# Kernel tuning notes

Hardware: AMD Instinct MI355X
Metric: run time of the kernel (lower is better)

## Reference

```python
import jax, jax.numpy as jnp
import numpy as np

D_MODEL = 1024
NUM_HEADS = 16
D_K = D_MODEL // NUM_HEADS  # 64
THETA = 10000.0
B = 2
L = 2048


def _rope(x, positions):
    # x: [B, H, L, d_k], positions: [B, L]
    half = D_K // 2
    freqs = 1.0 / (THETA ** (jnp.arange(0, D_K, 2, dtype=jnp.float32) / D_K))  # [half]
    angles = positions.astype(jnp.float32)[..., None] * freqs  # [B, L, half]
    cos = jnp.cos(angles)[:, None, :, :]  # [B, 1, L, half]
    sin = jnp.sin(angles)[:, None, :, :]
    x_even = x[..., 0::2]
    x_odd = x[..., 1::2]
    r_even = x_even * cos - x_odd * sin
    r_odd = x_even * sin + x_odd * cos
    # interleave back: [..., half, 2] -> [..., d_k]
    return jnp.stack([r_even, r_odd], axis=-1).reshape(x.shape)


def setup_inputs() -> dict:
    key = jax.random.key(0)
    ks = jax.random.split(key, 5)
    std = np.sqrt(2.0 / (D_MODEL + D_MODEL))
    x = jax.random.normal(ks[0], (B, L, D_MODEL), dtype=jnp.float32)
    token_positions = jnp.broadcast_to(jnp.arange(L, dtype=jnp.int64 if jax.config.jax_enable_x64 else jnp.int32), (B, L))
    WQ = jax.random.truncated_normal(ks[1], -3.0, 3.0, (D_MODEL, D_MODEL), dtype=jnp.float32) * std
    WK = jax.random.truncated_normal(ks[2], -3.0, 3.0, (D_MODEL, D_MODEL), dtype=jnp.float32) * std
    WV = jax.random.truncated_normal(ks[3], -3.0, 3.0, (D_MODEL, D_MODEL), dtype=jnp.float32) * std
    WO = jax.random.truncated_normal(ks[4], -3.0, 3.0, (D_MODEL, D_MODEL), dtype=jnp.float32) * std
    return {"x": x, "token_positions": token_positions, "WQ": WQ, "WK": WK, "WV": WV, "WO": WO}


def reference(x, token_positions, WQ, WK, WV, WO):
    # Projections: W is [out, in] -> y = x @ W.T
    Q = jnp.einsum('bld,ed->ble', x, WQ)
    K = jnp.einsum('bld,ed->ble', x, WK)
    V = jnp.einsum('bld,ed->ble', x, WV)
    # [B, L, H*d] -> [B, H, L, d]
    def split_heads(t):
        return t.reshape(B, L, NUM_HEADS, D_K).transpose(0, 2, 1, 3)
    Q, K, V = split_heads(Q), split_heads(K), split_heads(V)
    Q = _rope(Q, token_positions)
    K = _rope(K, token_positions)
    scores = jnp.einsum('bhqd,bhkd->bhqk', Q, K) / np.sqrt(D_K).astype(np.float32)
    causal = jnp.tril(jnp.ones((L, L), dtype=bool))
    scores = jnp.where(causal, scores, -jnp.inf)
    attn = jax.nn.softmax(scores, axis=-1)
    out = jnp.einsum('bhqk,bhkd->bhqd', attn, V)  # [B, H, L, d]
    out = out.transpose(0, 2, 1, 3).reshape(B, L, D_MODEL)
    return jnp.einsum('bld,ed->ble', out, WO)
```

## Files before the change

kernel.cpp:

```cpp
#include <hip/hip_runtime.h>
#include <cstdint>
#include <cstddef>

#define D_MODEL 1024
#define NHEAD   16
#define DKH     64
#define BATCH   2
#define SEQ     2048
#define BL      (BATCH*SEQ)

typedef unsigned short u16;
typedef unsigned int   u32;
typedef __bf16 bf16_t;
typedef bf16_t bf16x8 __attribute__((ext_vector_type(8)));
typedef u16    u16x8  __attribute__((ext_vector_type(8)));
typedef u32    u32x4  __attribute__((ext_vector_type(4)));
typedef float  f32x4  __attribute__((ext_vector_type(4)));
typedef float  f32x16 __attribute__((ext_vector_type(16)));

__device__ __forceinline__ u16 f2bf(float f) {
  u32 u = __builtin_bit_cast(u32, f);
  u32 r = (u + 0x7FFFu + ((u >> 16) & 1u)) >> 16;
  return (u16)r;
}
__device__ __forceinline__ float bf2f(u16 h) {
  u32 u = ((u32)h) << 16;
  return __builtin_bit_cast(float, u);
}
__device__ __forceinline__ bf16x8 ldb8(const u16* p) {
  return __builtin_bit_cast(bf16x8, *(const u16x8*)p);
}
__device__ __forceinline__ void gl_lds16(const u16* g, u16* l) {
  __builtin_amdgcn_global_load_lds((const __attribute__((address_space(1))) void*)g,
                                   (__attribute__((address_space(3))) void*)l, 16, 0, 0);
}
#define MFMA16x16x32(a,b,c) __builtin_amdgcn_mfma_f32_16x16x32_bf16((a),(b),(c),0,0,0)
#define MFMA32x32x16(a,b,c) __builtin_amdgcn_mfma_f32_32x32x16_bf16((a),(b),(c),0,0,0)

__global__ void __launch_bounds__(256) cvt1_kernel(const float* __restrict__ in, u16* __restrict__ out, int n8) {
  int i = blockIdx.x * 256 + threadIdx.x;
  if (i >= n8) return;
  float4 a = ((const float4*)in)[2*i];
  float4 b = ((const float4*)in)[2*i+1];
  u16x8 o;
  o[0]=f2bf(a.x); o[1]=f2bf(a.y); o[2]=f2bf(a.z); o[3]=f2bf(a.w);
  o[4]=f2bf(b.x); o[5]=f2bf(b.y); o[6]=f2bf(b.z); o[7]=f2bf(b.w);
  ((u16x8*)out)[i] = o;
}

__global__ void __launch_bounds__(256) cvt4_kernel(const float* __restrict__ i0, const float* __restrict__ i1,
                                                   const float* __restrict__ i2, const float* __restrict__ i3,
                                                   u16* __restrict__ o0, u16* __restrict__ o1,
                                                   u16* __restrict__ o2, u16* __restrict__ o3, int n8) {
  int i = blockIdx.x * 256 + threadIdx.x;
  if (i >= n8) return;
  const float* in = (blockIdx.y == 0) ? i0 : (blockIdx.y == 1) ? i1 : (blockIdx.y == 2) ? i2 : i3;
  u16*        out = (blockIdx.y == 0) ? o0 : (blockIdx.y == 1) ? o1 : (blockIdx.y == 2) ? o2 : o3;
  float4 a = ((const float4*)in)[2*i];
  float4 b = ((const float4*)in)[2*i+1];
  u16x8 o;
  o[0]=f2bf(a.x); o[1]=f2bf(a.y); o[2]=f2bf(a.z); o[3]=f2bf(a.w);
  o[4]=f2bf(b.x); o[5]=f2bf(b.y); o[6]=f2bf(b.z); o[7]=f2bf(b.w);
  ((u16x8*)out)[i] = o;
}

template<bool F32OUT>
__device__ __forceinline__ void gemm_body(const u16* __restrict__ A, const u16* __restrict__ W,
                                          void* __restrict__ Cv, int M, int N, int K,
                                          const int* __restrict__ pos, int mode) {
  __shared__ u16 Als[128*64];
  __shared__ u16 Bls[128*64];
  const int tid = threadIdx.x, lane = tid & 63, w = tid >> 6;
  const int wr = w >> 1, wc = w & 1;
  const int lr = lane & 15, lg = lane >> 4;
  const int m0 = blockIdx.x * 128, n0 = blockIdx.y * 128;
  f32x4 acc[4][4] = {};
  const int srow = lane >> 3;
  const int scol = (lane & 7) * 8;
  for (int k0 = 0; k0 < K; k0 += 64) {
    __syncthreads();
    #pragma unroll
    for (int c = 0; c < 4; ++c) {
      const int rb = w*32 + c*8;
      const u16* ga = A + (size_t)(m0 + rb + srow)*K + k0 + scol;
      const u16* gb = W + (size_t)(n0 + rb + srow)*K + k0 + scol;
      gl_lds16(ga, &Als[rb*64]);
      gl_lds16(gb, &Bls[rb*64]);
    }
    __syncthreads();
    #pragma unroll
    for (int ks = 0; ks < 2; ++ks) {
      bf16x8 am[4], bn[4];
      #pragma unroll
      for (int f = 0; f < 4; ++f) {
        am[f] = ldb8(&Als[(wr*64 + f*16 + lr)*64 + ks*32 + lg*8]);
        bn[f] = ldb8(&Bls[(wc*64 + f*16 + lr)*64 + ks*32 + lg*8]);
      }
      #pragma unroll
      for (int fm = 0; fm < 4; ++fm)
        #pragma unroll
        for (int fn = 0; fn < 4; ++fn)
          acc[fm][fn] = MFMA16x16x32(am[fm], bn[fn], acc[fm][fn]);
    }
  }
  if constexpr (!F32OUT) {
    if (mode) {
      const float QS  = 0.18033688011112042f;
      const float sgn = (lane & 1) ? 1.0f : -1.0f;
      float fr[4];
      #pragma unroll
      for (int fn = 0; fn < 4; ++fn)
        fr[fn] = exp2f(-(float)((fn*16 + lr) >> 1) * 0.41524101186092f);
      #pragma unroll
      for (int fm = 0; fm < 4; ++fm)
        #pragma unroll
        for (int r = 0; r < 4; ++r) {
          const int row = m0 + wr*64 + fm*16 + lg*4 + r;
          const float p = (float)pos[row];
          #pragma unroll
          for (int fn = 0; fn < 4; ++fn) {
            float sv, cv;
            __sincosf(p * fr[fn], &sv, &cv);
            float v  = acc[fm][fn][r];
            float vp = __shfl_xor(v, 1, 64);
            float out = v*cv + sgn*vp*sv;
            if (mode == 1) out *= QS;
            ((u16*)Cv)[(size_t)row*N + n0 + wc*64 + fn*16 + lr] = f2bf(out);
          }
        }
      return;
    }
  }
  #pragma unroll
  for (int fm = 0; fm < 4; ++fm)
    #pragma unroll
    for (int fn = 0; fn < 4; ++fn)
      #pragma unroll
      for (int r = 0; r < 4; ++r) {
        const int row = m0 + wr*64 + fm*16 + lg*4 + r;
        const int col = n0 + wc*64 + fn*16 + lr;
        if constexpr (F32OUT) ((float*)Cv)[(size_t)row*N + col] = acc[fm][fn][r];
        else                  ((u16*)Cv)[(size_t)row*N + col] = f2bf(acc[fm][fn][r]);
      }
}

__global__ void __launch_bounds__(256) gemm_qkv_kernel(const u16* __restrict__ X,
    const u16* __restrict__ Wq, const u16* __restrict__ Wk, const u16* __restrict__ Wv,
    u16* __restrict__ Qo, u16* __restrict__ Ko, u16* __restrict__ Vo,
    const int* __restrict__ pos) {
  const u16* W = (blockIdx.z == 0) ? Wq : (blockIdx.z == 1) ? Wk : Wv;
  u16*       C = (blockIdx.z == 0) ? Qo : (blockIdx.z == 1) ? Ko : Vo;
  const int mode = (blockIdx.z == 0) ? 1 : (blockIdx.z == 1) ? 2 : 0;
  gemm_body<false>(X, W, C, BL, D_MODEL, D_MODEL, pos, mode);
}

__global__ void __launch_bounds__(256) gemm_out_kernel(const u16* __restrict__ A, const u16* __restrict__ W,
                                                       float* __restrict__ C) {
  gemm_body<true>(A, W, C, BL, D_MODEL, D_MODEL, nullptr, 0);
}


struct AttnLds {
  union {
    struct { u16 K[2][2][64*64]; u16 V[2][2][64*64]; } s;
    float mg[4*64*34];
  } u;
};

__device__ __forceinline__ void attn_pass(
    const int q0, const int T,
    const u16* __restrict__ Qb, const u16* __restrict__ Kb,
    const u16* __restrict__ Vb, u16* __restrict__ Ob,
    AttnLds& sh, const int lane, const int w)
{
  const int wl = w & 3, isB = w >> 2;
  const int l31 = lane & 31, h32 = lane >> 5;
  const int SPLIT = T >> 1;
  const int qw0 = q0 + wl * 32;
  const int srow  = lane >> 3;
  const int scol8 = ((lane & 7) ^ srow) * 8;
  const int t0 = isB ? SPLIT : 0;
  const int vswz = (l31 & 7) << 3;

  bf16x8 qf[4];
  #pragma unroll
  for (int kc = 0; kc < 4; ++kc)
    qf[kc] = ldb8(Qb + (size_t)(qw0 + l31)*D_MODEL + kc*16 + h32*8);
  f32x16 o0 = {}, o1 = {};
  float mrun = 0.0f, lrun = 0.0f;

  {
    const int kv = t0 * 64;
    #pragma unroll
    for (int c = 0; c < 2; ++c) {
      const int rb = wl*16 + c*8;
      gl_lds16(Kb + (size_t)(kv + rb + srow)*D_MODEL + scol8, &sh.u.s.K[isB][0][rb*64]);
    }
    u16x8 a = *(const u16x8*)(Vb + (size_t)(kv + lane)*D_MODEL + (wl*2)*8);
    u16x8 c = *(const u16x8*)(Vb + (size_t)(kv + lane)*D_MODEL + (wl*2+1)*8);
    #pragma unroll
    for (int j = 0; j < 8; ++j) sh.u.s.V[isB][0][(wl*16 + j)*64 + (lane ^ (j<<3))] = a[j];
    #pragma unroll
    for (int j = 0; j < 8; ++j) sh.u.s.V[isB][0][(wl*16 + 8 + j)*64 + (lane ^ (j<<3))] = c[j];
  }
  __syncthreads();

  for (int i = 0; i < SPLIT; ++i) {
    const int buf = i & 1, nbuf = buf ^ 1;
    const bool pf = (i + 1 < SPLIT);
    u16x8 vr0, vr1;
    if (pf) {
      const int kvn = (t0 + i + 1) * 64;
      #pragma unroll
      for (int c = 0; c < 2; ++c) {
        const int rb = wl*16 + c*8;
        gl_lds16(Kb + (size_t)(kvn + rb + srow)*D_MODEL + scol8, &sh.u.s.K[isB][nbuf][rb*64]);
      }
      vr0 = *(const u16x8*)(Vb + (size_t)(kvn + lane)*D_MODEL + (wl*2)*8);
      vr1 = *(const u16x8*)(Vb + (size_t)(kvn + lane)*D_MODEL + (wl*2+1)*8);
    }
    const int kv0 = (t0 + i) * 64;
    if (kv0 <= qw0 + 31) {
      const u16* K0 = sh.u.s.K[isB][buf];
      const u16* V0 = sh.u.s.V[isB][buf];
      f32x16 s[2];
      #pragma unroll
      for (int r = 0; r < 16; ++r) { s[0][r] = -mrun; s[1][r] = -mrun; }
      #pragma unroll
      for (int kc = 0; kc < 4; ++kc) {
        const int sl = ((2*kc + h32) ^ (l31 & 7)) * 8;
        bf16x8 k0 = ldb8(&K0[(l31)*64 + sl]);
        bf16x8 k1 = ldb8(&K0[(32 + l31)*64 + sl]);
        s[0] = MFMA32x32x16(k0, qf[kc], s[0]);
        s[1] = MFMA32x32x16(k1, qf[kc], s[1]);
      }
      if (kv0 + 63 > qw0) {
        const int qrow = qw0 + l31;
        #pragma unroll
        for (int kb = 0; kb < 2; ++kb)
          #pragma unroll
          for (int r = 0; r < 16; ++r) {
            int kp = kv0 + kb*32 + (r&3) + 8*(r>>2) + 4*h32;
            if (kp > qrow) s[kb][r] = -1e30f;
          }
      }
      float t[16];
      #pragma unroll
      for (int j = 0; j < 16; ++j) t[j] = fmaxf(s[0][j], s[1][j]);
      #pragma unroll
      for (int st = 8; st >= 1; st >>= 1)
        #pragma unroll
        for (int j = 0; j < 16; ++j) if (j < st) t[j] = fmaxf(t[j], t[j + st]);
      float mx = t[0];
      mx = fmaxf(mx, __shfl_xor(mx, 32, 64));
      if (!__all(mx <= 8.0f)) {
        const float d  = fmaxf(mx, 0.0f);
        const float al = exp2f(-d);
        #pragma unroll
        for (int r = 0; r < 16; ++r) {
          float ar = __shfl(al, (r&3) + 8*(r>>2) + 4*h32, 64);
          o0[r] *= ar;
          o1[r] *= ar;
        }
        lrun *= al;
        mrun += d;
        #pragma unroll
        for (int kb = 0; kb < 2; ++kb)
          #pragma unroll
          for (int r = 0; r < 16; ++r) s[kb][r] -= d;
      }
      #pragma unroll
      for (int kb = 0; kb < 2; ++kb)
        #pragma unroll
        for (int r = 0; r < 16; ++r)
          s[kb][r] = exp2f(s[kb][r]);
      float us[16];
      #pragma unroll
      for (int j = 0; j < 16; ++j) us[j] = s[0][j] + s[1][j];
      #pragma unroll
      for (int st = 8; st >= 1; st >>= 1)
        #pragma unroll
        for (int j = 0; j < 16; ++j) if (j < st) us[j] += us[j + st];
      float ps = us[0];
      ps += __shfl_xor(ps, 32, 64);
      lrun += ps;
      #pragma unroll
      for (int kb = 0; kb < 2; ++kb) {
        u32 pk[8], sw[8];
        #pragma unroll
        for (int k2 = 0; k2 < 8; ++k2) {
          u32 pk_;
          float lo = s[kb][2*k2], hi = s[kb][2*k2+1];
          asm("v_cvt_pk_bf16_f32 %0, %1, %2" : "=v"(pk_) : "v"(lo), "v"(hi));
          pk[k2] = pk_;
          sw[k2] = (u32)__shfl_xor((int)pk_, 32, 64);
        }
        #pragma unroll
        for (int lm = 0; lm < 2; ++lm) {
          const int c = 2*kb + lm;
          u32x4 fw;
          fw[0] = h32 ? sw[4*lm+2] : pk[4*lm+0];
          fw[1] = h32 ? sw[4*lm+3] : pk[4*lm+1];
          fw[2] = h32 ? pk[4*lm+2] : sw[4*lm+0];
          fw[3] = h32 ? pk[4*lm+3] : sw[4*lm+1];
          bf16x8 pfr = __builtin_bit_cast(bf16x8, fw);
          bf16x8 v0 = ldb8(&V0[(l31)*64 + ((16*c + 8*h32) ^ vswz)]);
          bf16x8 v1 = ldb8(&V0[(32 + l31)*64 + ((16*c + 8*h32) ^ vswz)]);
          o0 = MFMA32x32x16(pfr, v0, o0);
          o1 = MFMA32x32x16(pfr, v1, o1);
        }
      }
    }
    if (pf) {
      u16* Vtn = sh.u.s.V[isB][nbuf];
      #pragma unroll
      for (int j = 0; j < 8; ++j) Vtn[(wl*16 + j)*64 + (lane ^ (j<<3))] = vr0[j];
      #pragma unroll
      for (int j = 0; j < 8; ++j) Vtn[(wl*16 + 8 + j)*64 + (lane ^ (j<<3))] = vr1[j];
    }
    __syncthreads();
  }
  float* mg = sh.u.mg;
  if (isB) {
    float* slot = mg + (size_t)(wl*64 + lane) * 34;
    #pragma unroll
    for (int r = 0; r < 16; ++r) { slot[r] = o0[r]; slot[16 + r] = o1[r]; }
    slot[32] = mrun; slot[33] = lrun;
  }
  __syncthreads();
  if (!isB) {
    const float* slot = mg + (size_t)(wl*64 + lane) * 34;
    const float mB = slot[32], lB = slot[33];
    const float m  = fmaxf(mrun, mB);
    const float eA = exp2f(mrun - m), eB = exp2f(mB - m);
    const float linv = 1.0f / (lrun * eA + lB * eB);
    #pragma unroll
    for (int r = 0; r < 16; ++r) {
      const int rp = (r&3) + 8*(r>>2) + 4*h32;
      const float eAr = __shfl(eA, rp, 64);
      const float eBr = __shfl(eB, rp, 64);
      const float lir = __shfl(linv, rp, 64);
      const float v0 = (o0[r]*eAr + slot[r]*eBr) * lir;
      const float v1 = (o1[r]*eAr + slot[16 + r]*eBr) * lir;
      const size_t grow = (size_t)(qw0 + rp) * D_MODEL;
      Ob[grow + l31]      = f2bf(v0);
      Ob[grow + 32 + l31] = f2bf(v1);
    }
  }
}

__global__ void __launch_bounds__(512) attn_kernel(const u16* __restrict__ Q, const u16* __restrict__ K,
                                                   const u16* __restrict__ V, u16* __restrict__ O) {
  __shared__ AttnLds sh;
  const int tid = threadIdx.x, lane = tid & 63, w = tid >> 6;
  const int n = blockIdx.x;
  const int bh = n & 31;
  const int q = 15 - (n >> 5);
  const int b = bh >> 4, head = bh & 15;
  const size_t headoff = (size_t)b * SEQ * D_MODEL + head * DKH;
  const u16* Qb = Q + headoff;
  const u16* Kb = K + headoff;
  const u16* Vb = V + headoff;
  u16* Ob = (u16*)O + headoff;
  attn_pass(q*128, 2*(q+1), Qb, Kb, Vb, Ob, sh, lane, w);
}

extern "C" void kernel_launch(void* const* d_in, const int* in_sizes, int n_in,
                              void* d_out, int out_size, void* d_ws, size_t ws_size,
                              hipStream_t stream) {
  const float* x  = (const float*)d_in[0];
  const int* pos  = (const int*)d_in[1];
  const float* WQ = (const float*)d_in[2];
  const float* WK = (const float*)d_in[3];
  const float* WV = (const float*)d_in[4];
  const float* WO = (const float*)d_in[5];
  u16* ws = (u16*)d_ws;
  const size_t NX = (size_t)BL * D_MODEL;
  const size_t NW = (size_t)D_MODEL * D_MODEL;
  u16* xb  = ws;
  u16* wqb = xb  + NX;
  u16* wkb = wqb + NW;
  u16* wvb = wkb + NW;
  u16* wob = wvb + NW;
  u16* qb  = wob + NW;
  u16* kb  = qb  + NX;
  u16* vb  = kb  + NX;
  u16* ab  = vb  + NX;

  cvt1_kernel<<<dim3((unsigned)(NX/8/256)), 256, 0, stream>>>(x, xb, (int)(NX/8));
  cvt4_kernel<<<dim3((unsigned)(NW/8/256), 4), 256, 0, stream>>>(WQ, WK, WV, WO, wqb, wkb, wvb, wob, (int)(NW/8));
  gemm_qkv_kernel<<<dim3(BL/128, D_MODEL/128, 3), 256, 0, stream>>>(xb, wqb, wkb, wvb, qb, kb, vb, pos);
  attn_kernel<<<dim3(512), 512, 0, stream>>>(qb, kb, vb, ab);
  gemm_out_kernel<<<dim3(BL/128, D_MODEL/128), 256, 0, stream>>>(ab, wob, (float*)d_out);
}
```

Before: 139.5 us.

## Double-buffer GEMM LDS tiles and precompute RoPE cos/sin table

Both projection GEMMs now use double-buffered LDS. The next K tile is loaded asynchronously while MFMAs run on the current one, and the loop needs only one barrier per step instead of two. The RoPE epilogue reads cos/sin from a table built by a new small kernel indexed by position, so it no longer calls exp2/sincos per element. This doubles shared memory per block (64KB), which may reduce occupancy, and adds one extra launch plus table reads from global memory.

```diff
diff --git a/kernel.cpp b/kernel.cpp
--- a/kernel.cpp
+++ b/kernel.cpp
@@ -64,12 +64,22 @@
   ((u16x8*)out)[i] = o;
 }
 
+__global__ void __launch_bounds__(256) rope_tab_kernel(float2* __restrict__ tab) {
+  int t = blockIdx.x * 256 + threadIdx.x;
+  int p = t >> 5, i = t & 31;
+  float fr = exp2f(-(float)i * 0.41524101186092f);
+  float sv, cv;
+  __sincosf((float)p * fr, &sv, &cv);
+  tab[t] = make_float2(cv, sv);
+}
+
 template<bool F32OUT>
 __device__ __forceinline__ void gemm_body(const u16* __restrict__ A, const u16* __restrict__ W,
                                           void* __restrict__ Cv, int M, int N, int K,
-                                          const int* __restrict__ pos, int mode) {
-  __shared__ u16 Als[128*64];
-  __shared__ u16 Bls[128*64];
+                                          const int* __restrict__ pos,
+                                          const float2* __restrict__ tab, int mode) {
+  __shared__ u16 Als[2][128*64];
+  __shared__ u16 Bls[2][128*64];
   const int tid = threadIdx.x, lane = tid & 63, w = tid >> 6;
   const int wr = w >> 1, wc = w & 1;
   const int lr = lane & 15, lg = lane >> 4;
@@ -77,24 +87,30 @@
   f32x4 acc[4][4] = {};
   const int srow = lane >> 3;
   const int scol = (lane & 7) * 8;
+  #pragma unroll
+  for (int c = 0; c < 4; ++c) {
+    const int rb = w*32 + c*8;
+    gl_lds16(A + (size_t)(m0 + rb + srow)*K + scol, &Als[0][rb*64]);
+    gl_lds16(W + (size_t)(n0 + rb + srow)*K + scol, &Bls[0][rb*64]);
+  }
+  __syncthreads();
   for (int k0 = 0; k0 < K; k0 += 64) {
-    __syncthreads();
-    #pragma unroll
-    for (int c = 0; c < 4; ++c) {
-      const int rb = w*32 + c*8;
-      const u16* ga = A + (size_t)(m0 + rb + srow)*K + k0 + scol;
-      const u16* gb = W + (size_t)(n0 + rb + srow)*K + k0 + scol;
-      gl_lds16(ga, &Als[rb*64]);
-      gl_lds16(gb, &Bls[rb*64]);
-    }
-    __syncthreads();
+    const int cur = (k0 >> 6) & 1, nxt = cur ^ 1;
+    if (k0 + 64 < K) {
+      #pragma unroll
+      for (int c = 0; c < 4; ++c) {
+        const int rb = w*32 + c*8;
+        gl_lds16(A + (size_t)(m0 + rb + srow)*K + k0 + 64 + scol, &Als[nxt][rb*64]);
+        gl_lds16(W + (size_t)(n0 + rb + srow)*K + k0 + 64 + scol, &Bls[nxt][rb*64]);
+      }
+    }
     #pragma unroll
     for (int ks = 0; ks < 2; ++ks) {
       bf16x8 am[4], bn[4];
       #pragma unroll
       for (int f = 0; f < 4; ++f) {
-        am[f] = ldb8(&Als[(wr*64 + f*16 + lr)*64 + ks*32 + lg*8]);
-        bn[f] = ldb8(&Bls[(wc*64 + f*16 + lr)*64 + ks*32 + lg*8]);
+        am[f] = ldb8(&Als[cur][(wr*64 + f*16 + lr)*64 + ks*32 + lg*8]);
+        bn[f] = ldb8(&Bls[cur][(wc*64 + f*16 + lr)*64 + ks*32 + lg*8]);
       }
       #pragma unroll
       for (int fm = 0; fm < 4; ++fm)
@@ -102,28 +118,24 @@
         for (int fn = 0; fn < 4; ++fn)
           acc[fm][fn] = MFMA16x16x32(am[fm], bn[fn], acc[fm][fn]);
     }
+    __syncthreads();
   }
   if constexpr (!F32OUT) {
     if (mode) {
       const float QS  = 0.18033688011112042f;
       const float sgn = (lane & 1) ? 1.0f : -1.0f;
-      float fr[4];
-      #pragma unroll
-      for (int fn = 0; fn < 4; ++fn)
-        fr[fn] = exp2f(-(float)((fn*16 + lr) >> 1) * 0.41524101186092f);
       #pragma unroll
       for (int fm = 0; fm < 4; ++fm)
         #pragma unroll
         for (int r = 0; r < 4; ++r) {
           const int row = m0 + wr*64 + fm*16 + lg*4 + r;
-          const float p = (float)pos[row];
+          const int p = pos[row];
           #pragma unroll
           for (int fn = 0; fn < 4; ++fn) {
-            float sv, cv;
-            __sincosf(p * fr[fn], &sv, &cv);
+            const float2 cs = tab[p*32 + fn*8 + (lr >> 1)];
             float v  = acc[fm][fn][r];
             float vp = __shfl_xor(v, 1, 64);
-            float out = v*cv + sgn*vp*sv;
+            float out = v*cs.x + sgn*vp*cs.y;
             if (mode == 1) out *= QS;
             ((u16*)Cv)[(size_t)row*N + n0 + wc*64 + fn*16 + lr] = f2bf(out);
           }
@@ -147,16 +159,16 @@
 __global__ void __launch_bounds__(256) gemm_qkv_kernel(const u16* __restrict__ X,
     const u16* __restrict__ Wq, const u16* __restrict__ Wk, const u16* __restrict__ Wv,
     u16* __restrict__ Qo, u16* __restrict__ Ko, u16* __restrict__ Vo,
-    const int* __restrict__ pos) {
+    const int* __restrict__ pos, const float2* __restrict__ tab) {
   const u16* W = (blockIdx.z == 0) ? Wq : (blockIdx.z == 1) ? Wk : Wv;
   u16*       C = (blockIdx.z == 0) ? Qo : (blockIdx.z == 1) ? Ko : Vo;
   const int mode = (blockIdx.z == 0) ? 1 : (blockIdx.z == 1) ? 2 : 0;
-  gemm_body<false>(X, W, C, BL, D_MODEL, D_MODEL, pos, mode);
+  gemm_body<false>(X, W, C, BL, D_MODEL, D_MODEL, pos, tab, mode);
 }
 
 __global__ void __launch_bounds__(256) gemm_out_kernel(const u16* __restrict__ A, const u16* __restrict__ W,
                                                        float* __restrict__ C) {
-  gemm_body<true>(A, W, C, BL, D_MODEL, D_MODEL, nullptr, 0);
+  gemm_body<true>(A, W, C, BL, D_MODEL, D_MODEL, nullptr, nullptr, 0);
 }
 
 
@@ -386,10 +398,12 @@
   u16* kb  = qb  + NX;
   u16* vb  = kb  + NX;
   u16* ab  = vb  + NX;
-
+  float2* tab = (float2*)(ab + NX);
+
+  rope_tab_kernel<<<dim3(SEQ*32/256), 256, 0, stream>>>(tab);
   cvt1_kernel<<<dim3((unsigned)(NX/8/256)), 256, 0, stream>>>(x, xb, (int)(NX/8));
   cvt4_kernel<<<dim3((unsigned)(NW/8/256), 4), 256, 0, stream>>>(WQ, WK, WV, WO, wqb, wkb, wvb, wob, (int)(NW/8));
-  gemm_qkv_kernel<<<dim3(BL/128, D_MODEL/128, 3), 256, 0, stream>>>(xb, wqb, wkb, wvb, qb, kb, vb, pos);
+  gemm_qkv_kernel<<<dim3(BL/128, D_MODEL/128, 3), 256, 0, stream>>>(xb, wqb, wkb, wvb, qb, kb, vb, pos, tab);
   attn_kernel<<<dim3(512), 512, 0, stream>>>(qb, kb, vb, ab);
   gemm_out_kernel<<<dim3(BL/128, D_MODEL/128), 256, 0, stream>>>(ab, wob, (float*)d_out);
 }
```

Result: slower. 146.0 us (+4.6%).
